# Kernel tuning notes

Hardware: AMD Instinct MI355X
Metric: run time of the kernel (lower is better)

## Reference

```python
import jax, jax.numpy as jnp
import numpy as np

EPS = 1e-5

def setup_inputs() -> dict:
    key = jax.random.key(0)
    B, N, F_in, F_out = 8, 2048, 64, 64
    ks = jax.random.split(key, 8)
    batch_nb_nodes = jax.random.randint(ks[0], (B,), N // 2, N + 1).astype(jnp.int32)
    node_mask = (jnp.arange(N)[None, :] < batch_nb_nodes[:, None]).astype(jnp.float32)  # [B,N]
    adj_mask = node_mask[:, :, None] * node_mask[:, None, :]                            # [B,N,N]
    emb_in = jax.random.normal(ks[1], (B, N, F_in), jnp.float32) * node_mask[:, :, None]
    adj_in = jax.random.uniform(ks[2], (B, N, N), jnp.float32) * adj_mask
    kernel_sigma = jnp.asarray(float(F_in), jnp.float32)          # gaussian kernel bandwidth
    combine_w = jnp.array([0.5, 0.5], jnp.float32)                # affine combine of [adj_in, kernel]
    conv_W = jax.random.normal(ks[3], (2 * F_in, F_out), jnp.float32) / np.float32(np.sqrt(2 * F_in))
    conv_b = jnp.zeros((F_out,), jnp.float32)
    nu_W = jax.random.normal(ks[4], (F_in + F_out, F_out), jnp.float32) / np.float32(np.sqrt(F_in + F_out))
    nu_b = jnp.zeros((F_out,), jnp.float32)
    return {"emb_in": emb_in, "adj_in": adj_in, "adj_mask": adj_mask,
            "batch_nb_nodes": batch_nb_nodes, "kernel_sigma": kernel_sigma,
            "combine_w": combine_w, "conv_W": conv_W, "conv_b": conv_b,
            "nu_W": nu_W, "nu_b": nu_b}

def reference(emb_in, adj_in, adj_mask, batch_nb_nodes, kernel_sigma, combine_w, conv_W, conv_b, nu_W, nu_b):
    B, N, F = emb_in.shape
    # --- gaussian kernel adjacency update: K_ij = exp(-||e_i - e_j||^2 / sigma) ---
    sq = jnp.sum(emb_in * emb_in, axis=-1)                                  # [B,N]
    d2 = sq[:, :, None] + sq[:, None, :] - 2.0 * jnp.einsum('bif,bjf->bij', emb_in, emb_in)
    ker = jnp.exp(-jnp.maximum(d2, 0.0) / kernel_sigma)                     # [B,N,N]
    # --- affine combine of previous adjacency and kernel matrices, then mask ---
    adj = (combine_w[0] * adj_in + combine_w[1] * ker) * adj_mask           # [B,N,N]
    # --- spatialnorm: per-graph mean/std over valid nodes (layer_nb != 0) ---
    node_mask = (jnp.arange(N)[None, :] < batch_nb_nodes[:, None]).astype(emb_in.dtype)  # [B,N]
    cnt = jnp.maximum(batch_nb_nodes.astype(emb_in.dtype), 1.0)[:, None, None]
    m = node_mask[:, :, None]
    mean = jnp.sum(emb_in * m, axis=1, keepdims=True) / cnt                 # [B,1,F]
    var = jnp.sum(((emb_in - mean) ** 2) * m, axis=1, keepdims=True) / cnt  # [B,1,F]
    emb_n = ((emb_in - mean) / jnp.sqrt(var + EPS)) * m                     # mask_embedding
    # --- operators: degree (D @ x) and adjacency (A @ x), joined then conv ---
    deg = jnp.sum(adj, axis=-1)                                             # [B,N]
    op_deg = deg[:, :, None] * emb_n                                        # [B,N,F]
    op_adj = jnp.einsum('bij,bjf->bif', adj, emb_n)                         # [B,N,F]
    emb_upd = jnp.concatenate([op_deg, op_adj], axis=-1) @ conv_W + conv_b  # [B,N,F_out]
    # --- node update: relu(W [emb_in ; emb_update] + b) ---
    emb = jax.nn.relu(jnp.concatenate([emb_in, emb_upd], axis=-1) @ nu_W + nu_b)
    return emb, adj
```

## Files before the change

kernel.cpp:

```cpp
#include <hip/hip_runtime.h>
#include <math.h>

#define BB 8
#define NN 2048
#define FF 64
#define EPSV 1e-5f
#define EMB_SZ (BB * NN * FF)

#define WS_SQ      0
#define WS_ASUM    (BB * NN)
#define WS_ASQ     (WS_ASUM + BB * FF)
#define WS_MEAN    (WS_ASQ + BB * FF)
#define WS_RSTD    (WS_MEAN + BB * FF)
#define WS_DEG     (WS_RSTD + BB * FF)
#define WS_F32_END (WS_DEG + BB * NN)

typedef __attribute__((ext_vector_type(8))) short bf16x8;
typedef __attribute__((ext_vector_type(4))) float f32x4;
typedef unsigned short ushort_t;

__device__ inline ushort_t f2bf(float x) {
    union { float f; unsigned u; } v; v.f = x;
    return (ushort_t)((v.u + 0x7fffu + ((v.u >> 16) & 1u)) >> 16);
}

__global__ __launch_bounds__(256) void k_stats(const float* __restrict__ emb,
                                               float* __restrict__ sq,
                                               float* __restrict__ asum,
                                               float* __restrict__ asq) {
    const int b    = blockIdx.y;
    const int lane = threadIdx.x & 63;
    const int grp  = threadIdx.x >> 6;
    const int base_i = blockIdx.x << 6;

    float s = 0.f, q = 0.f;
    for (int it = 0; it < 16; ++it) {
        const int i = base_i + (it << 2) + grp;
        const float x = emb[((size_t)(b * NN + i) << 6) + lane];
        const float x2 = x * x;
        s += x;
        q += x2;
        float r = x2;
        r += __shfl_xor(r, 1);
        r += __shfl_xor(r, 2);
        r += __shfl_xor(r, 4);
        r += __shfl_xor(r, 8);
        r += __shfl_xor(r, 16);
        r += __shfl_xor(r, 32);
        if (lane == 0) sq[b * NN + i] = r;
    }
    __shared__ float redS[4][64];
    __shared__ float redQ[4][64];
    redS[grp][lane] = s;
    redQ[grp][lane] = q;
    __syncthreads();
    if (threadIdx.x < 64) {
        const float ts = redS[0][lane] + redS[1][lane] + redS[2][lane] + redS[3][lane];
        const float tq = redQ[0][lane] + redQ[1][lane] + redQ[2][lane] + redQ[3][lane];
        atomicAdd(&asum[(b << 6) + lane], ts);
        atomicAdd(&asq[(b << 6) + lane], tq);
    }
}

__global__ void k_finalize(const float* __restrict__ asum, const float* __restrict__ asq,
                           const int* __restrict__ nbp,
                           float* __restrict__ mean, float* __restrict__ rstd) {
    const int t = threadIdx.x;
    const int b = t >> 6;
    const float cnt = fmaxf((float)nbp[b], 1.f);
    const float m = asum[t] / cnt;
    float v = asq[t] / cnt - m * m;
    v = fmaxf(v, 0.f);
    mean[t] = m;
    rstd[t] = rsqrtf(v + EPSV);
}

__global__ __launch_bounds__(256) void k_prep(const float* __restrict__ emb,
                                              const float* __restrict__ meanp,
                                              const float* __restrict__ rstdp,
                                              const int* __restrict__ nbp,
                                              ushort_t* __restrict__ embBf,
                                              ushort_t* __restrict__ embnT) {
    __shared__ __align__(16) ushort_t T[64][72];
    const int b = blockIdx.y, j0 = blockIdx.x << 6;
    const int nb = nbp[b], bN = b * NN;
    const int t = threadIdx.x;
    const int j = t >> 2, fs = (t & 3) << 4;

    float mn[16], rs[16];
#pragma unroll
    for (int e = 0; e < 16; e += 4) {
        *(float4*)&mn[e] = *(const float4*)(meanp + (b << 6) + fs + e);
        *(float4*)&rs[e] = *(const float4*)(rstdp + (b << 6) + fs + e);
    }
    const float msk = (j0 + j < nb) ? 1.f : 0.f;
    const float* src = emb + ((size_t)(bN + j0 + j) << 6) + fs;
    __align__(16) float x[16];
    *(float4*)(x + 0)  = *(const float4*)(src + 0);
    *(float4*)(x + 4)  = *(const float4*)(src + 4);
    *(float4*)(x + 8)  = *(const float4*)(src + 8);
    *(float4*)(x + 12) = *(const float4*)(src + 12);
    __align__(16) ushort_t raw[16];
#pragma unroll
    for (int e = 0; e < 16; ++e) {
        raw[e] = f2bf(x[e]);
        T[fs + e][j] = f2bf((x[e] - mn[e]) * rs[e] * msk);
    }
    ushort_t* dst = embBf + ((size_t)(bN + j0 + j) << 6) + fs;
    *(bf16x8*)dst       = *(bf16x8*)&raw[0];
    *(bf16x8*)(dst + 8) = *(bf16x8*)&raw[8];
    __syncthreads();
    const int f = t >> 2, js = (t & 3) << 4;
    const bf16x8 v0 = *(bf16x8*)&T[f][js];
    const bf16x8 v1 = *(bf16x8*)&T[f][js + 8];
    ushort_t* dstT = embnT + ((size_t)(b * FF + f) << 11) + j0 + js;
    *(bf16x8*)dstT       = v0;
    *(bf16x8*)(dstT + 8) = v1;
}

__global__ __launch_bounds__(256, 4) void k_adj(const ushort_t* __restrict__ embBf,
                                                const ushort_t* __restrict__ embnT,
                                                const float* __restrict__ adj_in,
                                                const float* __restrict__ sq,
                                                const float* __restrict__ sigp,
                                                const float* __restrict__ cw,
                                                const int* __restrict__ nbp,
                                                float* __restrict__ adj_out,
                                                float* __restrict__ deg,
                                                float* __restrict__ opadj) {
    __shared__ __align__(16) ushort_t BgA[8192];
    __shared__ __align__(16) ushort_t EnT[8192];

    const int b = blockIdx.z, i0 = blockIdx.y << 6, jbeg = blockIdx.x << 9;
    const int nb = nbp[b], bN = b * NN;
    const int tid = threadIdx.x, w = tid >> 6, lane = tid & 63;
    const int l15 = lane & 15, lq = lane >> 4;
    const int xk = (l15 & 7) << 4;
    const bool rowlive = (i0 < nb);
    const int nbr = (nb + 127) & ~127;
    const int jend = min(jbeg + 512, nbr);

    const float inv_sigma = 1.0f / sigp[0];
    const float w0 = cw[0], w1 = cw[1];

    const int ib = i0 + w * 16;
    bf16x8 ah0 = {}, ah1 = {};
    float sqi[4] = {0.f, 0.f, 0.f, 0.f};
    f32x4 accP[4];
#pragma unroll
    for (int c = 0; c < 4; ++c) accP[c] = (f32x4){0.f, 0.f, 0.f, 0.f};
    float rsum[4] = {0.f, 0.f, 0.f, 0.f};

    if (rowlive) {
        const ushort_t* ap = embBf + ((size_t)(bN + ib + l15) << 6) + lq * 8;
        ah0 = *(const bf16x8*)ap;
        ah1 = *(const bf16x8*)(ap + 32);
#pragma unroll
        for (int r = 0; r < 4; ++r) sqi[r] = sq[bN + ib + lq * 4 + r];
    }

    for (int jt = jbeg; jt < jbeg + 512; jt += 128) {
        if (rowlive && jt < jend) {
            {
                const int row = tid >> 1, fs2 = (tid & 1) << 5;
                const ushort_t* src = embBf + ((size_t)(bN + jt + row) << 6) + fs2;
                const int kx = (row & 7) << 4;
#pragma unroll
                for (int e = 0; e < 4; ++e) {
                    const bf16x8 v = *(const bf16x8*)(src + e * 8);
                    *(bf16x8*)((char*)BgA + (((row << 7) + ((fs2 + e * 8) << 1)) ^ kx)) = v;
                }
            }
            {
                const int f = tid >> 2, js = (tid & 3) << 5;
                const ushort_t* src = embnT + ((size_t)(b * FF + f) << 11) + jt + js;
                const int kx = (f & 7) << 4;
#pragma unroll
                for (int e = 0; e < 4; ++e) {
                    const bf16x8 v = *(const bf16x8*)(src + e * 8);
                    *(bf16x8*)((char*)EnT + (((f << 8) + ((js + e * 8) << 1)) ^ kx)) = v;
                }
            }
            __syncthreads();
            f32x4 acc[8];
#pragma unroll
            for (int c = 0; c < 8; ++c) acc[c] = (f32x4){0.f, 0.f, 0.f, 0.f};
#pragma unroll
            for (int c = 0; c < 8; ++c) {
                const int lin = ((c * 16 + l15) << 7) + lq * 16;
                const bf16x8 b0 = *(const bf16x8*)((char*)BgA + (lin ^ xk));
                const bf16x8 b1 = *(const bf16x8*)((char*)BgA + ((lin + 64) ^ xk));
                acc[c] = __builtin_amdgcn_mfma_f32_16x16x32_bf16(ah0, b0, acc[c], 0, 0, 0);
                acc[c] = __builtin_amdgcn_mfma_f32_16x16x32_bf16(ah1, b1, acc[c], 0, 0, 0);
            }
            float sqj[8];
#pragma unroll
            for (int c = 0; c < 8; ++c) sqj[c] = sq[bN + jt + c * 16 + l15];
#pragma unroll
            for (int r = 0; r < 4; ++r) {
                const int gi = ib + lq * 4 + r;
                const float mi = (gi < nb) ? 1.f : 0.f;
                const float* arow = adj_in + ((size_t)(bN + gi) << 11) + jt + l15;
                float* orow = adj_out + ((size_t)(bN + gi) << 11) + jt + l15;
#pragma unroll
                for (int c = 0; c < 8; ++c) {
                    const int gj = jt + c * 16 + l15;
                    float d2 = sqi[r] + sqj[c] - 2.f * acc[c][r];
                    d2 = fmaxf(d2, 0.f);
                    const float ker = __expf(-d2 * inv_sigma);
                    const float mv = (gj < nb) ? mi : 0.f;
                    const float o = (w0 * arow[c * 16] + w1 * ker) * mv;
                    orow[c * 16] = o;
                    acc[c][r] = o;
                    rsum[r] += o;
                }
            }
            __syncthreads();
#pragma unroll
            for (int r = 0; r < 4; ++r) {
                const int iloc = w * 16 + lq * 4 + r;
                const int kx2 = (iloc & 7) << 4;
#pragma unroll
                for (int c = 0; c < 8; ++c) {
                    const int lin = (iloc << 8) + ((c * 16 + l15) << 1);
                    *(ushort_t*)((char*)BgA + (lin ^ kx2)) = f2bf(acc[c][r]);
                }
            }
            __syncthreads();
#pragma unroll
            for (int ks = 0; ks < 4; ++ks) {
                const int lina = ((w * 16 + l15) << 8) + ks * 64 + lq * 16;
                const bf16x8 a = *(const bf16x8*)((char*)BgA + (lina ^ xk));
#pragma unroll
                for (int c = 0; c < 4; ++c) {
                    const int linb = ((c * 16 + l15) << 8) + ks * 64 + lq * 16;
                    const bf16x8 bv = *(const bf16x8*)((char*)EnT + (linb ^ xk));
                    accP[c] = __builtin_amdgcn_mfma_f32_16x16x32_bf16(a, bv, accP[c], 0, 0, 0);
                }
            }
            __syncthreads();
        } else {
            const float4 z = make_float4(0.f, 0.f, 0.f, 0.f);
#pragma unroll
            for (int q = 0; q < 8; ++q) {
                const int idx = tid * 8 + q;
                const int row = idx >> 5, c4 = (idx & 31) << 2;
                *(float4*)(adj_out + ((size_t)(bN + i0 + row) << 11) + jt + c4) = z;
            }
        }
    }

    if (rowlive) {
        const int irow = ib + lq * 4;
#pragma unroll
        for (int r = 0; r < 4; ++r) {
            float v = rsum[r];
            v += __shfl_xor(v, 1);
            v += __shfl_xor(v, 2);
            v += __shfl_xor(v, 4);
            v += __shfl_xor(v, 8);
            if (l15 == 0) atomicAdd(&deg[bN + irow + r], v);
        }
#pragma unroll
        for (int c = 0; c < 4; ++c)
#pragma unroll
            for (int r = 0; r < 4; ++r)
                atomicAdd(opadj + ((size_t)(bN + irow + r) << 6) + c * 16 + l15, accP[c][r]);
    }
}

__global__ __launch_bounds__(256) void k_epilogue(const float* __restrict__ emb,
                                                  const float* __restrict__ meanp,
                                                  const float* __restrict__ rstdp,
                                                  const float* __restrict__ degp,
                                                  const int* __restrict__ nbp,
                                                  const float* __restrict__ convW,
                                                  const float* __restrict__ convB,
                                                  const float* __restrict__ nuW,
                                                  const float* __restrict__ nuB,
                                                  float* __restrict__ emb_out) {
    __shared__ __align__(16) float smem[13056];
    float* xs = smem;
    float* us = smem + 8704;
    float* es = smem;

    const int b   = blockIdx.y;
    const int i0  = blockIdx.x << 6;
    const int tid = threadIdx.x;
    const int tx = tid & 15, ty = tid >> 4;
    const int nb = nbp[b];
    const int bN = b * NN;
    const int sj  = tid >> 2;
    const int scb = (tid & 3) << 4;

    {
        const float4 m4 = *(const float4*)(meanp + (b << 6) + (tx << 2));
        const float4 r4 = *(const float4*)(rstdp + (b << 6) + (tx << 2));
#pragma unroll
        for (int u = 0; u < 4; ++u) {
            const int il = (ty << 2) + u;
            const int gi = i0 + il;
            const float msk = (gi < nb) ? 1.f : 0.f;
            const float dg = degp[bN + gi];
            const float4 v = *(const float4*)(emb + ((size_t)(bN + gi) << 6) + (tx << 2));
            float4 en;
            en.x = (v.x - m4.x) * r4.x * msk;
            en.y = (v.y - m4.y) * r4.y * msk;
            en.z = (v.z - m4.z) * r4.z * msk;
            en.w = (v.w - m4.w) * r4.w * msk;
            float4 od;
            od.x = dg * en.x; od.y = dg * en.y; od.z = dg * en.z; od.w = dg * en.w;
            *(float4*)&xs[il * 132 + (tx << 2)] = od;
            const float4 oa = *(const float4*)(emb_out + ((size_t)(bN + gi) << 6) + (tx << 2));
            *(float4*)&xs[il * 132 + 64 + (tx << 2)] = oa;
        }
    }
    __syncthreads();

    {
        float u4[4][4];
#pragma unroll
        for (int r = 0; r < 4; ++r)
#pragma unroll
            for (int c = 0; c < 4; ++c) u4[r][c] = 0.f;
        for (int fis = 0; fis < 128; fis += 4) {
            const float4 w0v = *(const float4*)(convW + ((fis + 0) << 6) + (tx << 2));
            const float4 w1v = *(const float4*)(convW + ((fis + 1) << 6) + (tx << 2));
            const float4 w2v = *(const float4*)(convW + ((fis + 2) << 6) + (tx << 2));
            const float4 w3v = *(const float4*)(convW + ((fis + 3) << 6) + (tx << 2));
#pragma unroll
            for (int r = 0; r < 4; ++r) {
                const float4 x = *(const float4*)&xs[((ty << 2) + r) * 132 + fis];
                u4[r][0] += x.x * w0v.x + x.y * w1v.x + x.z * w2v.x + x.w * w3v.x;
                u4[r][1] += x.x * w0v.y + x.y * w1v.y + x.z * w2v.y + x.w * w3v.y;
                u4[r][2] += x.x * w0v.z + x.y * w1v.z + x.z * w2v.z + x.w * w3v.z;
                u4[r][3] += x.x * w0v.w + x.y * w1v.w + x.z * w2v.w + x.w * w3v.w;
            }
        }
        const float4 cb4 = *(const float4*)(convB + (tx << 2));
#pragma unroll
        for (int r = 0; r < 4; ++r) {
            float4 o;
            o.x = u4[r][0] + cb4.x; o.y = u4[r][1] + cb4.y;
            o.z = u4[r][2] + cb4.z; o.w = u4[r][3] + cb4.w;
            *(float4*)&us[((ty << 2) + r) * 68 + (tx << 2)] = o;
        }
    }
    __syncthreads();

    {
        const float* pe = emb + ((size_t)(bN + i0 + sj) << 6) + scb;
#pragma unroll
        for (int u = 0; u < 4; ++u)
            *(float4*)&es[sj * 68 + scb + (u << 2)] = *(const float4*)(pe + (u << 2));
    }
    __syncthreads();

    {
        float u4[4][4];
#pragma unroll
        for (int r = 0; r < 4; ++r)
#pragma unroll
            for (int c = 0; c < 4; ++c) u4[r][c] = 0.f;
        for (int fis = 0; fis < 64; fis += 4) {
            const float4 w0v = *(const float4*)(nuW + ((fis + 0) << 6) + (tx << 2));
            const float4 w1v = *(const float4*)(nuW + ((fis + 1) << 6) + (tx << 2));
            const float4 w2v = *(const float4*)(nuW + ((fis + 2) << 6) + (tx << 2));
            const float4 w3v = *(const float4*)(nuW + ((fis + 3) << 6) + (tx << 2));
#pragma unroll
            for (int r = 0; r < 4; ++r) {
                const float4 x = *(const float4*)&es[((ty << 2) + r) * 68 + fis];
                u4[r][0] += x.x * w0v.x + x.y * w1v.x + x.z * w2v.x + x.w * w3v.x;
                u4[r][1] += x.x * w0v.y + x.y * w1v.y + x.z * w2v.y + x.w * w3v.y;
                u4[r][2] += x.x * w0v.z + x.y * w1v.z + x.z * w2v.z + x.w * w3v.z;
                u4[r][3] += x.x * w0v.w + x.y * w1v.w + x.z * w2v.w + x.w * w3v.w;
            }
        }
        for (int fis = 0; fis < 64; fis += 4) {
            const float4 w0v = *(const float4*)(nuW + ((64 + fis + 0) << 6) + (tx << 2));
            const float4 w1v = *(const float4*)(nuW + ((64 + fis + 1) << 6) + (tx << 2));
            const float4 w2v = *(const float4*)(nuW + ((64 + fis + 2) << 6) + (tx << 2));
            const float4 w3v = *(const float4*)(nuW + ((64 + fis + 3) << 6) + (tx << 2));
#pragma unroll
            for (int r = 0; r < 4; ++r) {
                const float4 x = *(const float4*)&us[((ty << 2) + r) * 68 + fis];
                u4[r][0] += x.x * w0v.x + x.y * w1v.x + x.z * w2v.x + x.w * w3v.x;
                u4[r][1] += x.x * w0v.y + x.y * w1v.y + x.z * w2v.y + x.w * w3v.y;
                u4[r][2] += x.x * w0v.z + x.y * w1v.z + x.z * w2v.z + x.w * w3v.z;
                u4[r][3] += x.x * w0v.w + x.y * w1v.w + x.z * w2v.w + x.w * w3v.w;
            }
        }
        const float4 nb4 = *(const float4*)(nuB + (tx << 2));
#pragma unroll
        for (int r = 0; r < 4; ++r) {
            const int gi = i0 + (ty << 2) + r;
            float4 o;
            o.x = fmaxf(u4[r][0] + nb4.x, 0.f);
            o.y = fmaxf(u4[r][1] + nb4.y, 0.f);
            o.z = fmaxf(u4[r][2] + nb4.z, 0.f);
            o.w = fmaxf(u4[r][3] + nb4.w, 0.f);
            *(float4*)(emb_out + ((size_t)(bN + gi) << 6) + (tx << 2)) = o;
        }
    }
}

extern "C" void kernel_launch(void* const* d_in, const int* in_sizes, int n_in,
                              void* d_out, int out_size, void* d_ws, size_t ws_size,
                              hipStream_t stream) {
    (void)in_sizes; (void)n_in; (void)out_size; (void)ws_size;
    const float* emb_in   = (const float*)d_in[0];
    const float* adj_in   = (const float*)d_in[1];
    const int*   nbp      = (const int*)d_in[3];
    const float* sigp     = (const float*)d_in[4];
    const float* cw       = (const float*)d_in[5];
    const float* convW    = (const float*)d_in[6];
    const float* convB    = (const float*)d_in[7];
    const float* nuW      = (const float*)d_in[8];
    const float* nuB      = (const float*)d_in[9];

    float* emb_out = (float*)d_out;
    float* adj_out = (float*)d_out + EMB_SZ;

    float* ws   = (float*)d_ws;
    float* sq   = ws + WS_SQ;
    float* asum = ws + WS_ASUM;
    float* asq  = ws + WS_ASQ;
    float* mean = ws + WS_MEAN;
    float* rstd = ws + WS_RSTD;
    float* deg  = ws + WS_DEG;
    ushort_t* embBf = (ushort_t*)(ws + WS_F32_END);
    ushort_t* embnT = embBf + (size_t)BB * NN * FF;

    hipMemsetAsync(asum, 0, (WS_F32_END - WS_ASUM) * sizeof(float), stream);
    hipMemsetAsync(emb_out, 0, (size_t)EMB_SZ * sizeof(float), stream);

    k_stats<<<dim3(32, BB), 256, 0, stream>>>(emb_in, sq, asum, asq);
    k_finalize<<<1, BB * FF, 0, stream>>>(asum, asq, nbp, mean, rstd);
    k_prep<<<dim3(32, BB), 256, 0, stream>>>(emb_in, mean, rstd, nbp, embBf, embnT);
    k_adj<<<dim3(4, 32, BB), 256, 0, stream>>>(embBf, embnT, adj_in, sq, sigp, cw,
                                               nbp, adj_out, deg, emb_out);
    k_epilogue<<<dim3(32, BB), 256, 0, stream>>>(emb_in, mean, rstd, deg, nbp,
                                                 convW, convB, nuW, nuB, emb_out);
}
```

Measured before the change: 430.3 us.

## Split fused adjacency kernel into adjacency/degree and A@x kernels

```diff
diff --git a/kernel.cpp b/kernel.cpp
--- a/kernel.cpp
+++ b/kernel.cpp
@@ -118,155 +118,130 @@
     *(bf16x8*)(dstT + 8) = v1;
 }
 
-__global__ __launch_bounds__(256, 4) void k_adj(const ushort_t* __restrict__ embBf,
-                                                const ushort_t* __restrict__ embnT,
-                                                const float* __restrict__ adj_in,
-                                                const float* __restrict__ sq,
-                                                const float* __restrict__ sigp,
-                                                const float* __restrict__ cw,
-                                                const int* __restrict__ nbp,
-                                                float* __restrict__ adj_out,
-                                                float* __restrict__ deg,
-                                                float* __restrict__ opadj) {
-    __shared__ __align__(16) ushort_t BgA[8192];
-    __shared__ __align__(16) ushort_t EnT[8192];
-
-    const int b = blockIdx.z, i0 = blockIdx.y << 6, jbeg = blockIdx.x << 9;
+__global__ __launch_bounds__(256, 4) void k_adj_deg(const ushort_t* __restrict__ embBf,
+                                                    const float* __restrict__ adj_in,
+                                                    const float* __restrict__ sq,
+                                                    const float* __restrict__ sigp,
+                                                    const float* __restrict__ cw,
+                                                    const int* __restrict__ nbp,
+                                                    float* __restrict__ adj_out,
+                                                    float* __restrict__ deg) {
+    const int b = blockIdx.z, i0 = blockIdx.y << 6, j0 = blockIdx.x << 7;
     const int nb = nbp[b], bN = b * NN;
     const int tid = threadIdx.x, w = tid >> 6, lane = tid & 63;
     const int l15 = lane & 15, lq = lane >> 4;
-    const int xk = (l15 & 7) << 4;
-    const bool rowlive = (i0 < nb);
-    const int nbr = (nb + 127) & ~127;
-    const int jend = min(jbeg + 512, nbr);
+
+    if (i0 >= nb || j0 >= nb) {
+        const float4 z = make_float4(0.f, 0.f, 0.f, 0.f);
+#pragma unroll
+        for (int q = 0; q < 8; ++q) {
+            const int idx = (tid << 3) + q;
+            const int row = idx >> 5, c4 = (idx & 31) << 2;
+            *(float4*)(adj_out + ((size_t)(bN + i0 + row) << 11) + j0 + c4) = z;
+        }
+        return;
+    }
+
+    const int ib = i0 + w * 16;
+
+    float ain[4][8];
+#pragma unroll
+    for (int r = 0; r < 4; ++r) {
+        const float* arow = adj_in + ((size_t)(bN + ib + lq * 4 + r) << 11) + j0 + l15;
+#pragma unroll
+        for (int c = 0; c < 8; ++c) ain[r][c] = arow[c << 4];
+    }
+    float sqi[4], sqj[8];
+#pragma unroll
+    for (int r = 0; r < 4; ++r) sqi[r] = sq[bN + ib + lq * 4 + r];
+#pragma unroll
+    for (int c = 0; c < 8; ++c) sqj[c] = sq[bN + j0 + c * 16 + l15];
+
+    const ushort_t* ap = embBf + ((size_t)(bN + ib + l15) << 6) + lq * 8;
+    const bf16x8 a0 = *(const bf16x8*)ap;
+    const bf16x8 a1 = *(const bf16x8*)(ap + 32);
+
+    f32x4 acc[8];
+#pragma unroll
+    for (int c = 0; c < 8; ++c) acc[c] = (f32x4){0.f, 0.f, 0.f, 0.f};
+#pragma unroll
+    for (int c = 0; c < 8; ++c) {
+        const ushort_t* bp = embBf + ((size_t)(bN + j0 + c * 16 + l15) << 6) + lq * 8;
+        const bf16x8 b0 = *(const bf16x8*)bp;
+        const bf16x8 b1 = *(const bf16x8*)(bp + 32);
+        acc[c] = __builtin_amdgcn_mfma_f32_16x16x32_bf16(a0, b0, acc[c], 0, 0, 0);
+        acc[c] = __builtin_amdgcn_mfma_f32_16x16x32_bf16(a1, b1, acc[c], 0, 0, 0);
+    }
 
     const float inv_sigma = 1.0f / sigp[0];
     const float w0 = cw[0], w1 = cw[1];
-
-    const int ib = i0 + w * 16;
-    bf16x8 ah0 = {}, ah1 = {};
-    float sqi[4] = {0.f, 0.f, 0.f, 0.f};
-    f32x4 accP[4];
-#pragma unroll
-    for (int c = 0; c < 4; ++c) accP[c] = (f32x4){0.f, 0.f, 0.f, 0.f};
-    float rsum[4] = {0.f, 0.f, 0.f, 0.f};
-
-    if (rowlive) {
-        const ushort_t* ap = embBf + ((size_t)(bN + ib + l15) << 6) + lq * 8;
-        ah0 = *(const bf16x8*)ap;
-        ah1 = *(const bf16x8*)(ap + 32);
-#pragma unroll
-        for (int r = 0; r < 4; ++r) sqi[r] = sq[bN + ib + lq * 4 + r];
-    }
-
-    for (int jt = jbeg; jt < jbeg + 512; jt += 128) {
-        if (rowlive && jt < jend) {
-            {
-                const int row = tid >> 1, fs2 = (tid & 1) << 5;
-                const ushort_t* src = embBf + ((size_t)(bN + jt + row) << 6) + fs2;
-                const int kx = (row & 7) << 4;
-#pragma unroll
-                for (int e = 0; e < 4; ++e) {
-                    const bf16x8 v = *(const bf16x8*)(src + e * 8);
-                    *(bf16x8*)((char*)BgA + (((row << 7) + ((fs2 + e * 8) << 1)) ^ kx)) = v;
-                }
-            }
-            {
-                const int f = tid >> 2, js = (tid & 3) << 5;
-                const ushort_t* src = embnT + ((size_t)(b * FF + f) << 11) + jt + js;
-                const int kx = (f & 7) << 4;
-#pragma unroll
-                for (int e = 0; e < 4; ++e) {
-                    const bf16x8 v = *(const bf16x8*)(src + e * 8);
-                    *(bf16x8*)((char*)EnT + (((f << 8) + ((js + e * 8) << 1)) ^ kx)) = v;
-                }
-            }
-            __syncthreads();
-            f32x4 acc[8];
-#pragma unroll
-            for (int c = 0; c < 8; ++c) acc[c] = (f32x4){0.f, 0.f, 0.f, 0.f};
-#pragma unroll
-            for (int c = 0; c < 8; ++c) {
-                const int lin = ((c * 16 + l15) << 7) + lq * 16;
-                const bf16x8 b0 = *(const bf16x8*)((char*)BgA + (lin ^ xk));
-                const bf16x8 b1 = *(const bf16x8*)((char*)BgA + ((lin + 64) ^ xk));
-                acc[c] = __builtin_amdgcn_mfma_f32_16x16x32_bf16(ah0, b0, acc[c], 0, 0, 0);
-                acc[c] = __builtin_amdgcn_mfma_f32_16x16x32_bf16(ah1, b1, acc[c], 0, 0, 0);
-            }
-            float sqj[8];
-#pragma unroll
-            for (int c = 0; c < 8; ++c) sqj[c] = sq[bN + jt + c * 16 + l15];
-#pragma unroll
-            for (int r = 0; r < 4; ++r) {
-                const int gi = ib + lq * 4 + r;
-                const float mi = (gi < nb) ? 1.f : 0.f;
-                const float* arow = adj_in + ((size_t)(bN + gi) << 11) + jt + l15;
-                float* orow = adj_out + ((size_t)(bN + gi) << 11) + jt + l15;
-#pragma unroll
-                for (int c = 0; c < 8; ++c) {
-                    const int gj = jt + c * 16 + l15;
-                    float d2 = sqi[r] + sqj[c] - 2.f * acc[c][r];
-                    d2 = fmaxf(d2, 0.f);
-                    const float ker = __expf(-d2 * inv_sigma);
-                    const float mv = (gj < nb) ? mi : 0.f;
-                    const float o = (w0 * arow[c * 16] + w1 * ker) * mv;
-                    orow[c * 16] = o;
-                    acc[c][r] = o;
-                    rsum[r] += o;
-                }
-            }
-            __syncthreads();
-#pragma unroll
-            for (int r = 0; r < 4; ++r) {
-                const int iloc = w * 16 + lq * 4 + r;
-                const int kx2 = (iloc & 7) << 4;
-#pragma unroll
-                for (int c = 0; c < 8; ++c) {
-                    const int lin = (iloc << 8) + ((c * 16 + l15) << 1);
-                    *(ushort_t*)((char*)BgA + (lin ^ kx2)) = f2bf(acc[c][r]);
-                }
-            }
-            __syncthreads();
-#pragma unroll
-            for (int ks = 0; ks < 4; ++ks) {
-                const int lina = ((w * 16 + l15) << 8) + ks * 64 + lq * 16;
-                const bf16x8 a = *(const bf16x8*)((char*)BgA + (lina ^ xk));
-#pragma unroll
-                for (int c = 0; c < 4; ++c) {
-                    const int linb = ((c * 16 + l15) << 8) + ks * 64 + lq * 16;
-                    const bf16x8 bv = *(const bf16x8*)((char*)EnT + (linb ^ xk));
-                    accP[c] = __builtin_amdgcn_mfma_f32_16x16x32_bf16(a, bv, accP[c], 0, 0, 0);
-                }
-            }
-            __syncthreads();
-        } else {
-            const float4 z = make_float4(0.f, 0.f, 0.f, 0.f);
-#pragma unroll
-            for (int q = 0; q < 8; ++q) {
-                const int idx = tid * 8 + q;
-                const int row = idx >> 5, c4 = (idx & 31) << 2;
-                *(float4*)(adj_out + ((size_t)(bN + i0 + row) << 11) + jt + c4) = z;
-            }
-        }
-    }
-
-    if (rowlive) {
-        const int irow = ib + lq * 4;
+#pragma unroll
+    for (int r = 0; r < 4; ++r) {
+        const int gi = ib + lq * 4 + r;
+        const float mi = (gi < nb) ? 1.f : 0.f;
+        float* orow = adj_out + ((size_t)(bN + gi) << 11) + j0 + l15;
+        float rsum = 0.f;
+#pragma unroll
+        for (int c = 0; c < 8; ++c) {
+            const int gj = j0 + c * 16 + l15;
+            float d2 = sqi[r] + sqj[c] - 2.f * acc[c][r];
+            d2 = fmaxf(d2, 0.f);
+            const float ker = __expf(-d2 * inv_sigma);
+            const float mv = (gj < nb) ? mi : 0.f;
+            const float o = (w0 * ain[r][c] + w1 * ker) * mv;
+            orow[c << 4] = o;
+            rsum += o;
+        }
+        rsum += __shfl_xor(rsum, 1);
+        rsum += __shfl_xor(rsum, 2);
+        rsum += __shfl_xor(rsum, 4);
+        rsum += __shfl_xor(rsum, 8);
+        if (l15 == 0) atomicAdd(&deg[bN + gi], rsum);
+    }
+}
+
+__global__ __launch_bounds__(256, 4) void k_opadj(const float* __restrict__ adj,
+                                                  const ushort_t* __restrict__ embnT,
+                                                  const int* __restrict__ nbp,
+                                                  float* __restrict__ opadj) {
+    const int b = blockIdx.z, i0 = blockIdx.x << 6, jbeg = blockIdx.y << 9;
+    const int nb = nbp[b];
+    if (i0 >= nb || jbeg >= nb) return;
+    const int bN = b * NN;
+    const int jend = min(jbeg + 512, (nb + 31) & ~31);
+
+    const int tid = threadIdx.x, w = tid >> 6, lane = tid & 63;
+    const int l15 = lane & 15, lq = lane >> 4;
+
+    const float* arow = adj + ((size_t)(bN + i0 + w * 16 + l15) << 11);
+    const ushort_t* bbase = embnT + ((size_t)(b * FF + l15) << 11);
+
+    f32x4 acc[4];
+#pragma unroll
+    for (int c = 0; c < 4; ++c) acc[c] = (f32x4){0.f, 0.f, 0.f, 0.f};
+
+    for (int jt = jbeg; jt < jend; jt += 32) {
+        const float* ap = arow + jt + lq * 8;
+        const float4 x0 = *(const float4*)ap;
+        const float4 x1 = *(const float4*)(ap + 4);
+        __align__(16) ushort_t af[8];
+        af[0] = f2bf(x0.x); af[1] = f2bf(x0.y); af[2] = f2bf(x0.z); af[3] = f2bf(x0.w);
+        af[4] = f2bf(x1.x); af[5] = f2bf(x1.y); af[6] = f2bf(x1.z); af[7] = f2bf(x1.w);
+        const bf16x8 a = *(bf16x8*)af;
+#pragma unroll
+        for (int c = 0; c < 4; ++c) {
+            const bf16x8 bv = *(const bf16x8*)(bbase + ((size_t)(c * 16) << 11) + jt + lq * 8);
+            acc[c] = __builtin_amdgcn_mfma_f32_16x16x32_bf16(a, bv, acc[c], 0, 0, 0);
+        }
+    }
+
+#pragma unroll
+    for (int c = 0; c < 4; ++c)
 #pragma unroll
         for (int r = 0; r < 4; ++r) {
-            float v = rsum[r];
-            v += __shfl_xor(v, 1);
-            v += __shfl_xor(v, 2);
-            v += __shfl_xor(v, 4);
-            v += __shfl_xor(v, 8);
-            if (l15 == 0) atomicAdd(&deg[bN + irow + r], v);
-        }
-#pragma unroll
-        for (int c = 0; c < 4; ++c)
-#pragma unroll
-            for (int r = 0; r < 4; ++r)
-                atomicAdd(opadj + ((size_t)(bN + irow + r) << 6) + c * 16 + l15, accP[c][r]);
-    }
+            const int gi = i0 + w * 16 + lq * 4 + r;
+            atomicAdd(opadj + ((size_t)(bN + gi) << 6) + c * 16 + l15, acc[c][r]);
+        }
 }
 
 __global__ __launch_bounds__(256) void k_epilogue(const float* __restrict__ emb,
@@ -437,8 +412,9 @@
     k_stats<<<dim3(32, BB), 256, 0, stream>>>(emb_in, sq, asum, asq);
     k_finalize<<<1, BB * FF, 0, stream>>>(asum, asq, nbp, mean, rstd);
     k_prep<<<dim3(32, BB), 256, 0, stream>>>(emb_in, mean, rstd, nbp, embBf, embnT);
-    k_adj<<<dim3(4, 32, BB), 256, 0, stream>>>(embBf, embnT, adj_in, sq, sigp, cw,
-                                               nbp, adj_out, deg, emb_out);
+    k_adj_deg<<<dim3(NN / 128, NN / 64, BB), 256, 0, stream>>>(embBf, adj_in, sq, sigp,
+                                                               cw, nbp, adj_out, deg);
+    k_opadj<<<dim3(NN / 64, 4, BB), 256, 0, stream>>>(adj_out, embnT, nbp, emb_out);
     k_epilogue<<<dim3(32, BB), 256, 0, stream>>>(emb_in, mean, rstd, deg, nbp,
                                                  convW, convB, nuW, nuB, emb_out);
 }
```

Result: faster. 409.6 us (-4.8%).
